# Optimization experiments

Hardware: AMD Instinct MI355X
Metric: run time of the kernel (lower is better)

The kernel has to match this reference:

```python
import jax, jax.numpy as jnp
import numpy as np

NUM_HEADS = 16
ROPE_BASE = 2048.0


def _rope_tables(seq_len, head_dim, dtype):
    inv_freq = 1.0 / (ROPE_BASE ** (jnp.arange(0, head_dim, 2, dtype=jnp.float32) / head_dim))
    t = jnp.arange(seq_len, dtype=jnp.float32)
    freqs = jnp.einsum('i,j->ij', t, inv_freq)          # [N, D/2]
    emb = jnp.concatenate([freqs, freqs], axis=-1)       # [N, D]
    return jnp.cos(emb).astype(dtype), jnp.sin(emb).astype(dtype)


def _rotate_half(x):
    x1, x2 = jnp.split(x, 2, axis=-1)
    return jnp.concatenate([-x2, x1], axis=-1)


def setup_inputs() -> dict:
    key = jax.random.key(0)
    k1, k2, k3, k4 = jax.random.split(key, 4)
    B, N, C = 2, 2048, 1024
    x = jax.random.normal(k1, (B, N, C), dtype=jnp.float32)
    w_qkv = jax.random.normal(k2, (3 * C, C), dtype=jnp.float32) * (C ** -0.5)
    w_proj = jax.random.normal(k3, (C, C), dtype=jnp.float32) * (C ** -0.5)
    b_proj = jnp.zeros((C,), dtype=jnp.float32)
    key_padding_mask = jax.random.randint(k4, (B, N), 0, 2, dtype=jnp.int32)
    return {"x": x, "w_qkv": w_qkv, "w_proj": w_proj, "b_proj": b_proj,
            "key_padding_mask": key_padding_mask}


def reference(x, w_qkv, w_proj, b_proj, key_padding_mask):
    B, N, C = x.shape
    H = NUM_HEADS
    D = C // H
    scale = D ** -0.5

    qkv = x @ w_qkv.T                                    # [B, N, 3C]
    q, k, v = jnp.split(qkv, 3, axis=-1)
    # [B, N, C] -> [B, H, N, D]
    q = q.reshape(B, N, H, D).transpose(0, 2, 1, 3)
    k = k.reshape(B, N, H, D).transpose(0, 2, 1, 3)
    v = v.reshape(B, N, H, D).transpose(0, 2, 1, 3)

    cos, sin = _rope_tables(N, D, x.dtype)               # [N, D]
    q = q * cos + _rotate_half(q) * sin
    k = k * cos + _rotate_half(k) * sin

    attn = jnp.einsum('bhqd,bhkd->bhqk', q, k) * scale   # [B, H, N, N]
    mask = (key_padding_mask == 0)[:, None, None, :]     # [B, 1, 1, N]
    attn = jnp.where(mask, jnp.asarray(-1e9, attn.dtype), attn)
    attn = jax.nn.softmax(attn, axis=-1)

    out = jnp.einsum('bhqk,bhkd->bhqd', attn, v)         # [B, H, N, D]
    out = out.transpose(0, 2, 1, 3).reshape(B, N, C)
    return out @ w_proj.T + b_proj
```

## Files before the change

### kernel.cpp

```cpp
#include <hip/hip_runtime.h>


typedef __attribute__((ext_vector_type(8))) short          s16x8;
typedef __attribute__((ext_vector_type(8))) unsigned short u16x8;
typedef __attribute__((ext_vector_type(4))) unsigned short u16x4;
typedef __attribute__((ext_vector_type(4))) float          f32x4;
typedef __attribute__((ext_vector_type(16))) float         f32x16;
typedef __attribute__((ext_vector_type(4))) unsigned int   u32x4;

#define MFMA_BF16(a, b, c) __builtin_amdgcn_mfma_f32_16x16x32_bf16((a), (b), (c), 0, 0, 0)
#define MFMA32_BF16(a, b, c) __builtin_amdgcn_mfma_f32_32x32x16_bf16((a), (b), (c), 0, 0, 0)

#define GLD_TO_LDS(gp, lp) __builtin_amdgcn_global_load_lds(                  \
    (const __attribute__((address_space(1))) void*)(gp),                      \
    (__attribute__((address_space(3))) void*)(lp), 16, 0, 0)

__device__ __forceinline__ unsigned short f2bf(float f) {
    union { float f; unsigned int u; } v; v.f = f;
    unsigned int u = v.u;
    unsigned int r = u + 0x7FFFu + ((u >> 16) & 1u);
    return (unsigned short)(r >> 16);
}
__device__ __forceinline__ float bf2f(unsigned short h) {
    union { unsigned int u; float f; } v; v.u = ((unsigned int)h) << 16;
    return v.f;
}
__device__ __forceinline__ f32x16 zero16() {
    f32x16 z;
#pragma unroll
    for (int i = 0; i < 16; i++) z[i] = 0.f;
    return z;
}
__device__ __forceinline__ unsigned int pkbf(float a, float b) {
    return __builtin_amdgcn_perm(__builtin_bit_cast(unsigned int, b),
                                 __builtin_bit_cast(unsigned int, a), 0x07060302u);
}
__device__ __forceinline__ int perm16(int p) {
    return (p & 3) + 8 * ((p >> 2) & 1) + 4 * (p >> 3);
}

__global__ __launch_bounds__(256) void prep(const float* __restrict__ x,
                                            const float* __restrict__ wqkv,
                                            const float* __restrict__ wproj,
                                            const int* __restrict__ m,
                                            unsigned short* __restrict__ xb,
                                            unsigned short* __restrict__ wqkvb,
                                            unsigned short* __restrict__ wprojb,
                                            unsigned short* __restrict__ mb) {
    int blk = blockIdx.x, tid = threadIdx.x;
    if (blk < 4096) {
        const float* src; unsigned short* dst; int i;
        if (blk < 2048)      { src = x;     dst = xb;     i = blk * 256 + tid; }
        else if (blk < 3584) { src = wqkv;  dst = wqkvb;  i = (blk - 2048) * 256 + tid; }
        else                 { src = wproj; dst = wprojb; i = (blk - 3584) * 256 + tid; }
        f32x4 v0 = ((const f32x4*)src)[i * 2];
        f32x4 v1 = ((const f32x4*)src)[i * 2 + 1];
        u16x8 o;
        o[0] = f2bf(v0[0]); o[1] = f2bf(v0[1]); o[2] = f2bf(v0[2]); o[3] = f2bf(v0[3]);
        o[4] = f2bf(v1[0]); o[5] = f2bf(v1[1]); o[6] = f2bf(v1[2]); o[7] = f2bf(v1[3]);
        ((u16x8*)dst)[i] = o;
    } else {
        int i = (blk - 4096) * 256 + tid;
        int src = (i & ~15) | perm16(i & 15);
        mb[i] = (m[src] == 0) ? (unsigned short)0 : (unsigned short)0x3F80;
    }
}

__global__ __launch_bounds__(256) void gemm_bt(const unsigned short* __restrict__ A,
                                               const unsigned short* __restrict__ B,
                                               unsigned short* __restrict__ C,
                                               unsigned short* __restrict__ Km,
                                               int M, int N, int K) {
    __shared__ unsigned short Al[128][64];
    __shared__ unsigned short Bl[128][64];
    const int tid  = threadIdx.x;
    const int lane = tid & 63;
    const int qd   = lane >> 4;
    const int cc   = lane & 15;
    const int wave = tid >> 6;
    const int wr   = wave >> 1, wc = wave & 1;
    const int nbx  = N >> 7;
    const int nwg  = gridDim.x;
    int d = blockIdx.x;
    int s = (nwg % 8 == 0) ? (d % 8) * (nwg / 8) + d / 8 : d;
    const int m0   = (s / nbx) * 128, n0 = (s % nbx) * 128;
    unsigned short* Alf = &Al[0][0];
    unsigned short* Blf = &Bl[0][0];

    f32x4 acc[4][4];
#pragma unroll
    for (int i = 0; i < 4; i++)
#pragma unroll
        for (int j = 0; j < 4; j++) acc[i][j] = (f32x4){0.f, 0.f, 0.f, 0.f};

    for (int k0 = 0; k0 < K; k0 += 64) {
#pragma unroll
        for (int t = 0; t < 4; t++) {
            int idx = t * 256 + tid;
            int row = idx >> 3, sg = (idx & 7) ^ (row & 7);
            GLD_TO_LDS(A + (size_t)(m0 + row) * K + k0 + sg * 8, Alf + idx * 8);
            GLD_TO_LDS(B + (size_t)(n0 + row) * K + k0 + sg * 8, Blf + idx * 8);
        }
        __syncthreads();
#pragma unroll
        for (int ks = 0; ks < 64; ks += 32) {
            const int s4 = ks >> 3;
            s16x8 af[4], bf[4];
#pragma unroll
            for (int i = 0; i < 4; i++) {
                int r = wr * 64 + i * 16 + cc;
                af[i] = *(const s16x8*)&Al[r][((s4 + qd) ^ (r & 7)) * 8];
            }
#pragma unroll
            for (int j = 0; j < 4; j++) {
                int r = wc * 64 + j * 16 + cc;
                bf[j] = *(const s16x8*)&Bl[r][((s4 + qd) ^ (r & 7)) * 8];
            }
#pragma unroll
            for (int i = 0; i < 4; i++)
#pragma unroll
                for (int j = 0; j < 4; j++)
                    acc[i][j] = MFMA_BF16(af[i], bf[j], acc[i][j]);
        }
        __syncthreads();
    }
    if (n0 >= 1024 && n0 < 2048) {
#pragma unroll
        for (int i = 0; i < 4; i++)
#pragma unroll
            for (int r = 0; r < 4; r++) {
                int row = m0 + wr * 64 + i * 16 + qd * 4 + r;
                int bb = row >> 11, n = row & 2047;
                float cth[2], sth[2];
#pragma unroll
                for (int p2 = 0; p2 < 2; p2++) {
                    float th = (float)n * exp2f(-0.34375f * (float)(p2 * 16 + cc));
                    cth[p2] = __cosf(th); sth[p2] = __sinf(th);
                }
#pragma unroll
                for (int j = 0; j < 4; j++) {
                    int kcol = n0 - 1024 + wc * 64 + j * 16 + cc;
                    int h = kcol >> 6, dd2 = kcol & 63;
                    float sgn = (j < 2) ? -1.0f : 1.0f;
                    float v = acc[i][j][r], p = acc[i][j ^ 2][r];
                    Km[((size_t)(bb * 16 + h) * 2048 + n) * 64 + dd2] =
                        f2bf(v * cth[j & 1] + sgn * p * sth[j & 1]);
                }
            }
    } else {
#pragma unroll
        for (int i = 0; i < 4; i++)
#pragma unroll
            for (int j = 0; j < 4; j++)
#pragma unroll
                for (int r = 0; r < 4; r++) {
                    int row = m0 + wr * 64 + i * 16 + qd * 4 + r;
                    int col = n0 + wc * 64 + j * 16 + cc;
                    C[(size_t)row * N + col] = f2bf(acc[i][j][r]);
                }
    }
}

__global__ __launch_bounds__(256) void v_scatter(const unsigned short* __restrict__ qkv,
                                                 const int* __restrict__ msk,
                                                 unsigned short* __restrict__ Vt) {
    const int N = 2048, H = 16, D = 64, C3 = 3072;
    __shared__ unsigned short vl[64][65];
    const int nt = blockIdx.x, h = blockIdx.y, b = blockIdx.z;
    const int n0 = nt * 64;
    const int tid = threadIdx.x;
    const size_t bh = (size_t)b * H + h;
#pragma unroll
    for (int it = 0; it < 2; it++) {
        int idx = tid + it * 256;
        int row = idx >> 3, seg = idx & 7;
        int d0 = seg * 8;
        int n = n0 + row;
        int keep = msk[(size_t)b * N + n];
        u16x8 vv = *(const u16x8*)&qkv[((size_t)b * N + n) * C3 + 2048 + h * 64 + d0];
#pragma unroll
        for (int j = 0; j < 8; j++) vl[row][d0 + j] = keep ? vv[j] : (unsigned short)0;
    }
    __syncthreads();
#pragma unroll
    for (int it = 0; it < 2; it++) {
        int idx = tid + it * 256;
        int drow = idx >> 3, nseg = idx & 7;
        u16x8 ov;
#pragma unroll
        for (int j = 0; j < 8; j++) {
            int cpos = nseg * 8 + j;
            int srcl = (cpos & ~15) | perm16(cpos & 15);
            ov[j] = vl[srcl][drow];
        }
        *(u16x8*)&Vt[(bh * D + drow) * N + n0 + nseg * 8] = ov;
    }
}

__global__ __launch_bounds__(256, 2) void flash_attn(const unsigned short* __restrict__ qkvp,
                                                     const unsigned short* __restrict__ Kg,
                                                     const unsigned short* __restrict__ Vt,
                                                     const unsigned short* __restrict__ mb,
                                                     unsigned short* __restrict__ Og) {
    const int N = 2048, H = 16, D = 64;
    const float SCL = 0.18033688f;
    __shared__ unsigned short ldsbuf[4 * 64 * 64];
    unsigned short (*Kl0)[64] = (unsigned short(*)[64])(ldsbuf);
    unsigned short (*Kl1)[64] = (unsigned short(*)[64])(ldsbuf + 4096);
    unsigned short (*Vl0)[64] = (unsigned short(*)[64])(ldsbuf + 8192);
    unsigned short (*Vl1)[64] = (unsigned short(*)[64])(ldsbuf + 12288);
    const int tid  = threadIdx.x;
    const int lane = tid & 63;
    const int wave = tid >> 6;
    const int qhalf = wave & 1;
    const int khalf = wave >> 1;
    const int c    = lane & 31;
    const int hi   = lane >> 5;
    int dd = blockIdx.x;
    int sw = (dd & 7) * 64 + (dd >> 3);
    const int qt = sw & 15, h = (sw >> 4) & 15, b = sw >> 8;
    const int q0 = qt * 128;
    const size_t bh = (size_t)b * H + h;

    s16x8 qf[2][4];
    {
        s16x8 qraw[2][4];
#pragma unroll
        for (int qs = 0; qs < 2; qs++) {
            const unsigned short* Qb =
                qkvp + ((size_t)b * N + q0 + qhalf * 64 + qs * 32 + c) * 3072 + h * 64;
#pragma unroll
            for (int kd = 0; kd < 4; kd++)
                qraw[qs][kd] = *(const s16x8*)(Qb + kd * 16 + hi * 8);
        }
#pragma unroll
        for (int qs = 0; qs < 2; qs++) {
            float nn = (float)(q0 + qhalf * 64 + qs * 32 + c);
#pragma unroll
            for (int kd = 0; kd < 4; kd++) {
                float sgn = (kd < 2) ? -1.0f : 1.0f;
#pragma unroll
                for (int j = 0; j < 8; j++) {
                    int jj = (kd & 1) * 16 + hi * 8 + j;
                    float th = nn * exp2f(-0.34375f * (float)jj);
                    float cth = __cosf(th), sth = __sinf(th);
                    float v = bf2f((unsigned short)qraw[qs][kd][j]);
                    float p = bf2f((unsigned short)qraw[qs][kd ^ 2][j]);
                    qf[qs][kd][j] = (short)f2bf((v * cth + sgn * p * sth) * SCL);
                }
            }
        }
    }

    f32x16 o[2][2], lacc[2];
#pragma unroll
    for (int qs = 0; qs < 2; qs++) {
        o[qs][0] = zero16(); o[qs][1] = zero16(); lacc[qs] = zero16();
    }

    const unsigned short* Kbase = Kg + bh * N * D;
    const unsigned short* Vbase = Vt + bh * D * N;
    const unsigned short* mbase = mb + (size_t)b * N;
    const int row_s = tid >> 3, sg_s = (tid & 7) ^ ((tid >> 3) & 7);
    const int row_s2 = (tid + 256) >> 3, sg_s2 = (tid & 7) ^ (((tid + 256) >> 3) & 7);

    auto issue = [&](int k0, unsigned short* Kb, unsigned short* Vb) {
        GLD_TO_LDS(Kbase + (size_t)(k0 + row_s) * D + sg_s * 8,   Kb + tid * 8);
        GLD_TO_LDS(Vbase + (size_t)row_s * N + k0 + sg_s * 8,     Vb + tid * 8);
        GLD_TO_LDS(Kbase + (size_t)(k0 + row_s2) * D + sg_s2 * 8, Kb + (tid + 256) * 8);
        GLD_TO_LDS(Vbase + (size_t)row_s2 * N + k0 + sg_s2 * 8,   Vb + (tid + 256) * 8);
    };

    auto compute = [&](int k0, const unsigned short (*Kb)[64], const unsigned short (*Vb)[64]) {
        auto packkg = [&](const f32x16& sstv, s16x8* pa) {
            float p[16];
#pragma unroll
            for (int r = 0; r < 16; r++) p[r] = __builtin_amdgcn_exp2f(sstv[r]);
#pragma unroll
            for (int half = 0; half < 2; half++) {
                int bs = half * 8;
                u32x4 w = { pkbf(p[bs + 0], p[bs + 1]), pkbf(p[bs + 2], p[bs + 3]),
                            pkbf(p[bs + 4], p[bs + 5]), pkbf(p[bs + 6], p[bs + 7]) };
                pa[half] = __builtin_bit_cast(s16x8, w);
            }
        };

        int kr = khalf * 32 + c;
        s16x8 kf[4];
#pragma unroll
        for (int kd = 0; kd < 4; kd++)
            kf[kd] = *(const s16x8*)&Kb[kr][((kd * 2 + hi) ^ (kr & 7)) * 8];
        f32x16 sst0 = zero16(), sst1 = zero16();
        __builtin_amdgcn_s_setprio(1);
#pragma unroll
        for (int kd = 0; kd < 4; kd++) {
            sst0 = MFMA32_BF16(kf[kd], qf[0][kd], sst0);
            sst1 = MFMA32_BF16(kf[kd], qf[1][kd], sst1);
        }
        __builtin_amdgcn_s_setprio(0);
        s16x8 pa[2][2];
        packkg(sst0, pa[0]);
        packkg(sst1, pa[1]);

#pragma unroll
        for (int ksl = 0; ksl < 2; ksl++) {
            int ks = khalf * 2 + ksl;
            s16x8 mfr = *(const s16x8*)&mbase[k0 + ks * 16 + hi * 8];
            int vr0 = c, vr1 = 32 + c;
            s16x8 vf0 = *(const s16x8*)&Vb[vr0][((ks * 2 + hi) ^ (vr0 & 7)) * 8];
            s16x8 vf1 = *(const s16x8*)&Vb[vr1][((ks * 2 + hi) ^ (vr1 & 7)) * 8];
            __builtin_amdgcn_s_setprio(1);
#pragma unroll
            for (int qs = 0; qs < 2; qs++) {
                lacc[qs]  = MFMA32_BF16(pa[qs][ksl], mfr, lacc[qs]);
                o[qs][0]  = MFMA32_BF16(pa[qs][ksl], vf0, o[qs][0]);
                o[qs][1]  = MFMA32_BF16(pa[qs][ksl], vf1, o[qs][1]);
            }
            __builtin_amdgcn_s_setprio(0);
        }
    };

    issue(0, &Kl0[0][0], &Vl0[0][0]);
    __syncthreads();
    for (int it = 0; it < 32; it += 2) {
        int k0 = it * 64;
        if (it + 1 < 32) issue(k0 + 64, &Kl1[0][0], &Vl1[0][0]);
        compute(k0, Kl0, Vl0);
        __syncthreads();
        if (it + 2 < 32) issue(k0 + 128, &Kl0[0][0], &Vl0[0][0]);
        compute(k0 + 64, Kl1, Vl1);
        __syncthreads();
    }

    float* red = (float*)ldsbuf;
#pragma unroll
    for (int qs = 0; qs < 2; qs++) {
        __syncthreads();
        if (khalf == 1) {
            float* dst = red + qhalf * 3136 + lane * 49;
#pragma unroll
            for (int r = 0; r < 16; r++) {
                dst[r] = o[qs][0][r]; dst[16 + r] = o[qs][1][r]; dst[32 + r] = lacc[qs][r];
            }
        }
        __syncthreads();
        if (khalf == 0) {
            const float* src = red + qhalf * 3136 + lane * 49;
#pragma unroll
            for (int r = 0; r < 16; r++) {
                o[qs][0][r] += src[r]; o[qs][1][r] += src[16 + r]; lacc[qs][r] += src[32 + r];
            }
        }
    }

    if (khalf == 0) {
#pragma unroll
        for (int qs = 0; qs < 2; qs++) {
            float linv[16];
#pragma unroll
            for (int r = 0; r < 16; r++) linv[r] = 1.0f / lacc[qs][r];
#pragma unroll
            for (int db = 0; db < 2; db++)
#pragma unroll
                for (int r = 0; r < 16; r++) {
                    int n = q0 + qhalf * 64 + qs * 32 + (r & 3) + 8 * (r >> 2) + 4 * hi;
                    Og[((size_t)b * N + n) * 1024 + h * 64 + db * 32 + c] =
                        f2bf(o[qs][db][r] * linv[r]);
                }
        }
    }
}

__global__ __launch_bounds__(256) void gemm_proj(const unsigned short* __restrict__ A,
                                                 const unsigned short* __restrict__ B,
                                                 float* __restrict__ C,
                                                 const float* __restrict__ bias) {
    const int NN = 1024, K = 1024;
    __shared__ unsigned short Al[128][64];
    __shared__ unsigned short Bl[64][64];
    const int tid  = threadIdx.x;
    const int lane = tid & 63;
    const int qd   = lane >> 4;
    const int cc   = lane & 15;
    const int wave = tid >> 6;
    const int wr   = wave >> 1, wc = wave & 1;
    int dd = blockIdx.x;
    int sw = (dd & 7) * 64 + (dd >> 3);
    const int m0   = (sw >> 4) * 128, n0 = (sw & 15) * 64;
    unsigned short* Alf = &Al[0][0];
    unsigned short* Blf = &Bl[0][0];

    f32x4 acc[4][2];
#pragma unroll
    for (int i = 0; i < 4; i++)
#pragma unroll
        for (int j = 0; j < 2; j++) acc[i][j] = (f32x4){0.f, 0.f, 0.f, 0.f};

    for (int k0 = 0; k0 < K; k0 += 64) {
#pragma unroll
        for (int t = 0; t < 4; t++) {
            int idx = t * 256 + tid;
            int row = idx >> 3, sg = (idx & 7) ^ (row & 7);
            GLD_TO_LDS(A + (size_t)(m0 + row) * K + k0 + sg * 8, Alf + idx * 8);
        }
#pragma unroll
        for (int t = 0; t < 2; t++) {
            int idx = t * 256 + tid;
            int row = idx >> 3, sg = (idx & 7) ^ (row & 7);
            GLD_TO_LDS(B + (size_t)(n0 + row) * K + k0 + sg * 8, Blf + idx * 8);
        }
        __syncthreads();
#pragma unroll
        for (int ks = 0; ks < 64; ks += 32) {
            const int s4 = ks >> 3;
            s16x8 af[4], bf[2];
#pragma unroll
            for (int i = 0; i < 4; i++) {
                int r = wr * 64 + i * 16 + cc;
                af[i] = *(const s16x8*)&Al[r][((s4 + qd) ^ (r & 7)) * 8];
            }
#pragma unroll
            for (int j = 0; j < 2; j++) {
                int r = wc * 32 + j * 16 + cc;
                bf[j] = *(const s16x8*)&Bl[r][((s4 + qd) ^ (r & 7)) * 8];
            }
#pragma unroll
            for (int i = 0; i < 4; i++)
#pragma unroll
                for (int j = 0; j < 2; j++)
                    acc[i][j] = MFMA_BF16(af[i], bf[j], acc[i][j]);
        }
        __syncthreads();
    }
#pragma unroll
    for (int i = 0; i < 4; i++)
#pragma unroll
        for (int j = 0; j < 2; j++)
#pragma unroll
            for (int r = 0; r < 4; r++) {
                int row = m0 + wr * 64 + i * 16 + qd * 4 + r;
                int col = n0 + wc * 32 + j * 16 + cc;
                C[(size_t)row * NN + col] = acc[i][j][r] + bias[col];
            }
}

extern "C" void kernel_launch(void* const* d_in, const int* in_sizes, int n_in,
                              void* d_out, int out_size, void* d_ws, size_t ws_size,
                              hipStream_t stream) {
    const float* x      = (const float*)d_in[0];
    const float* w_qkv  = (const float*)d_in[1];
    const float* w_proj = (const float*)d_in[2];
    const float* b_proj = (const float*)d_in[3];
    const int*   mask   = (const int*)d_in[4];
    float* out = (float*)d_out;

    unsigned short* ws     = (unsigned short*)d_ws;
    unsigned short* xb     = ws;
    unsigned short* wqkvb  = xb     + (size_t)4096 * 1024;
    unsigned short* wprojb = wqkvb  + (size_t)3072 * 1024;
    unsigned short* qkv    = wprojb + (size_t)1024 * 1024;
    unsigned short* Qm     = qkv    + (size_t)4096 * 3072;
    unsigned short* Km     = Qm     + (size_t)32 * 2048 * 64;
    unsigned short* Vtm    = Km     + (size_t)32 * 2048 * 64;
    unsigned short* attno  = Vtm    + (size_t)32 * 2048 * 64;
    unsigned short* maskbf = attno  + (size_t)4096 * 1024;

    prep<<<4112, 256, 0, stream>>>(x, w_qkv, w_proj, mask, xb, wqkvb, wprojb, maskbf);
    gemm_bt<<<768, 256, 0, stream>>>(xb, wqkvb, qkv, Km, 4096, 3072, 1024);
    v_scatter<<<dim3(32, 16, 2), 256, 0, stream>>>(qkv, mask, Vtm);
    flash_attn<<<512, 256, 0, stream>>>(qkv, Km, Vtm, maskbf, attno);
    gemm_proj<<<512, 256, 0, stream>>>(attno, wprojb, out, b_proj);
}
```

Baseline: 179.1 us.

## Fuse V masking and transpose into QKV GEMM epilogue, drop v_scatter kernel

The QKV GEMM epilogue for V columns now applies the key padding mask, stages the tile in an enlarged shared buffer, and writes V directly in transposed, permuted layout. This removes the separate v_scatter launch and its reread of V from the qkv buffer. In exchange the GEMM uses more LDS, which may lower occupancy, and V tiles get an extra sync and strided LDS reads in the epilogue.

```diff
diff --git a/kernel.cpp b/kernel.cpp
--- a/kernel.cpp
+++ b/kernel.cpp
@@ -68,11 +68,14 @@
 
 __global__ __launch_bounds__(256) void gemm_bt(const unsigned short* __restrict__ A,
                                                const unsigned short* __restrict__ B,
+                                               const int* __restrict__ msk,
                                                unsigned short* __restrict__ C,
                                                unsigned short* __restrict__ Km,
+                                               unsigned short* __restrict__ Vt,
                                                int M, int N, int K) {
-    __shared__ unsigned short Al[128][64];
-    __shared__ unsigned short Bl[128][64];
+    __shared__ unsigned short sbuf[128 * 130];
+    unsigned short (*Al)[64] = (unsigned short(*)[64])(sbuf);
+    unsigned short (*Bl)[64] = (unsigned short(*)[64])(sbuf + 128 * 64);
     const int tid  = threadIdx.x;
     const int lane = tid & 63;
     const int qd   = lane >> 4;
@@ -124,7 +127,37 @@
         }
         __syncthreads();
     }
-    if (n0 >= 1024 && n0 < 2048) {
+    if (n0 >= 2048) {
+        const int bb = m0 >> 11, tok0 = m0 & 2047;
+#pragma unroll
+        for (int i = 0; i < 4; i++)
+#pragma unroll
+            for (int r = 0; r < 4; r++) {
+                int tl = wr * 64 + i * 16 + qd * 4 + r;
+                int keep = msk[(size_t)bb * 2048 + tok0 + tl];
+#pragma unroll
+                for (int j = 0; j < 4; j++) {
+                    int cl = wc * 64 + j * 16 + cc;
+                    sbuf[tl * 130 + cl] = keep ? f2bf(acc[i][j][r]) : (unsigned short)0;
+                }
+            }
+        __syncthreads();
+#pragma unroll
+        for (int it = 0; it < 8; it++) {
+            int idx = it * 256 + tid;
+            int dr = idx >> 4, seg = idx & 15;
+            int col = n0 - 2048 + dr;
+            int gh = col >> 6, dd2 = col & 63;
+            u16x8 ov;
+#pragma unroll
+            for (int j = 0; j < 8; j++) {
+                int cpos = seg * 8 + j;
+                int srcl = (cpos & ~15) | perm16(cpos & 15);
+                ov[j] = sbuf[srcl * 130 + dr];
+            }
+            *(u16x8*)&Vt[((size_t)(bb * 16 + gh) * 64 + dd2) * 2048 + tok0 + seg * 8] = ov;
+        }
+    } else if (n0 >= 1024) {
 #pragma unroll
         for (int i = 0; i < 4; i++)
 #pragma unroll
@@ -158,42 +191,6 @@
                     int col = n0 + wc * 64 + j * 16 + cc;
                     C[(size_t)row * N + col] = f2bf(acc[i][j][r]);
                 }
-    }
-}
-
-__global__ __launch_bounds__(256) void v_scatter(const unsigned short* __restrict__ qkv,
-                                                 const int* __restrict__ msk,
-                                                 unsigned short* __restrict__ Vt) {
-    const int N = 2048, H = 16, D = 64, C3 = 3072;
-    __shared__ unsigned short vl[64][65];
-    const int nt = blockIdx.x, h = blockIdx.y, b = blockIdx.z;
-    const int n0 = nt * 64;
-    const int tid = threadIdx.x;
-    const size_t bh = (size_t)b * H + h;
-#pragma unroll
-    for (int it = 0; it < 2; it++) {
-        int idx = tid + it * 256;
-        int row = idx >> 3, seg = idx & 7;
-        int d0 = seg * 8;
-        int n = n0 + row;
-        int keep = msk[(size_t)b * N + n];
-        u16x8 vv = *(const u16x8*)&qkv[((size_t)b * N + n) * C3 + 2048 + h * 64 + d0];
-#pragma unroll
-        for (int j = 0; j < 8; j++) vl[row][d0 + j] = keep ? vv[j] : (unsigned short)0;
-    }
-    __syncthreads();
-#pragma unroll
-    for (int it = 0; it < 2; it++) {
-        int idx = tid + it * 256;
-        int drow = idx >> 3, nseg = idx & 7;
-        u16x8 ov;
-#pragma unroll
-        for (int j = 0; j < 8; j++) {
-            int cpos = nseg * 8 + j;
-            int srcl = (cpos & ~15) | perm16(cpos & 15);
-            ov[j] = vl[srcl][drow];
-        }
-        *(u16x8*)&Vt[(bh * D + drow) * N + n0 + nseg * 8] = ov;
     }
 }
 
@@ -466,8 +463,7 @@
     unsigned short* maskbf = attno  + (size_t)4096 * 1024;
 
     prep<<<4112, 256, 0, stream>>>(x, w_qkv, w_proj, mask, xb, wqkvb, wprojb, maskbf);
-    gemm_bt<<<768, 256, 0, stream>>>(xb, wqkvb, qkv, Km, 4096, 3072, 1024);
-    v_scatter<<<dim3(32, 16, 2), 256, 0, stream>>>(qkv, mask, Vtm);
+    gemm_bt<<<768, 256, 0, stream>>>(xb, wqkvb, mask, qkv, Km, Vtm, 4096, 3072, 1024);
     flash_attn<<<512, 256, 0, stream>>>(qkv, Km, Vtm, maskbf, attno);
     gemm_proj<<<512, 256, 0, stream>>>(attno, wprojb, out, b_proj);
 }
```

Result: no change. 176.8 us (-1.3%).
